# Optimization experiments

Hardware: AMD Instinct MI355X
Metric: run time of the kernel (lower is better)

The kernel has to match this reference:

```python
import jax, jax.numpy as jnp
import numpy as np

B, T, C, H = 128, 256, 384, 6
D = C // H  # head dim = 64


def setup_inputs() -> dict:
    key = jax.random.key(0)
    k1, k2, k3, k4, k5 = jax.random.split(key, 5)
    s = 0.02
    return {
        "x": jax.random.normal(k1, (B, T, C), dtype=jnp.float32),
        "W_qkv": jax.random.normal(k2, (C, 3 * C), dtype=jnp.float32) * s,
        "b_qkv": jax.random.normal(k3, (3 * C,), dtype=jnp.float32) * s,
        "W_proj": jax.random.normal(k4, (C, C), dtype=jnp.float32) * s,
        "b_proj": jax.random.normal(k5, (C,), dtype=jnp.float32) * s,
    }


def reference(x, W_qkv, b_qkv, W_proj, b_proj):
    Bv, Tv, Cv = x.shape
    # fused QKV projection, then split
    qkv = x @ W_qkv + b_qkv                      # [B,T,3C]
    q, k, v = jnp.split(qkv, 3, axis=-1)
    # [B,T,C] -> [B,H,T,D]
    q = q.reshape(Bv, Tv, H, D).transpose(0, 2, 1, 3)
    k = k.reshape(Bv, Tv, H, D).transpose(0, 2, 1, 3)
    v = v.reshape(Bv, Tv, H, D).transpose(0, 2, 1, 3)
    # causal masked scores, scaled by head_dim**-0.5
    scores = jnp.einsum("bhqd,bhkd->bhqk", q, k) * (D ** -0.5)
    causal = jnp.tril(jnp.ones((Tv, Tv), dtype=bool))
    scores = jnp.where(causal, scores, -jnp.inf)
    wt = jax.nn.softmax(scores, axis=-1)
    # dropout layers are identity in eval mode
    out = jnp.einsum("bhqk,bhkd->bhqd", wt, v)   # [B,H,T,D]
    out = out.transpose(0, 2, 1, 3).reshape(Bv, Tv, Cv)
    return out @ W_proj + b_proj
```

## Files before the change

kernel.cpp:

```cpp
#include <hip/hip_runtime.h>

typedef unsigned short u16;
typedef unsigned int u32;
typedef __attribute__((ext_vector_type(4))) float f32x4;
typedef __attribute__((ext_vector_type(8))) __bf16 bf16x8;
typedef __attribute__((ext_vector_type(2))) __bf16 bf16x2;

#define NEGINF (-1e30f)
#define QSCALE 0.18033688011112042f

__device__ __forceinline__ u16 f32_to_bf16(float f) {
  union { float f; unsigned int u; } v;
  v.f = f;
  unsigned int u = v.u;
  u += 0x7fffu + ((u >> 16) & 1u);
  return (u16)(u >> 16);
}

__device__ __forceinline__ u32 pk_bf16(float a, float b) {
  bf16x2 t;
  t.x = (__bf16)a;
  t.y = (__bf16)b;
  return __builtin_bit_cast(u32, t);
}

__device__ __forceinline__ f32x4 mfma_bf16(bf16x8 a, bf16x8 b, f32x4 c) {
  return __builtin_amdgcn_mfma_f32_16x16x32_bf16(a, b, c, 0, 0, 0);
}

#define GLOAD_LDS16(g, l) __builtin_amdgcn_global_load_lds( \
    (const __attribute__((address_space(1))) unsigned int*)(g), \
    (__attribute__((address_space(3))) unsigned int*)(l), 16, 0, 0)

__global__ void k_cvt4(const float4* __restrict__ in, u16* __restrict__ out, int nq) {
  int i = blockIdx.x * blockDim.x + threadIdx.x;
  if (i >= nq) return;
  float4 v = in[i];
  uint2 o;
  o.x = (unsigned int)f32_to_bf16(v.x) | ((unsigned int)f32_to_bf16(v.y) << 16);
  o.y = (unsigned int)f32_to_bf16(v.z) | ((unsigned int)f32_to_bf16(v.w) << 16);
  *(uint2*)(out + (size_t)i * 4) = o;
}

__global__ void k_tcvt(const float* __restrict__ in, u16* __restrict__ out, int K, int N) {
  int idx = blockIdx.x * blockDim.x + threadIdx.x;
  if (idx >= K * N) return;
  int k = idx / N, n = idx - k * N;
  out[(size_t)n * K + k] = f32_to_bf16(in[idx]);
}

__device__ __forceinline__ void gemm256x64(
    const u16* __restrict__ A, const u16* __restrict__ Bt,
    int mBase, int nBase, u16* lsA, u16* lsB,
    f32x4 acc[4][2], int lane, int wv, int wm, int wn) {
  const int l15 = lane & 15;
  size_t aoff[4];
  u32 aldso[4];
#pragma unroll
  for (int jj = 0; jj < 4; ++jj) {
    int c = wv * 256 + jj * 64 + lane;
    int row = c >> 3;
    int kc = (c & 7) ^ (row & 7);
    aoff[jj] = (size_t)(mBase + row) * 384 + kc * 8;
    aldso[jj] = (u32)(wv * 256 + jj * 64) * 8;
  }
  int cb = wv * 64 + lane;
  int brow = cb >> 3;
  size_t boff = (size_t)(nBase + brow) * 384 + (size_t)(((cb & 7) ^ (brow & 7)) * 8);
  u32 bldso = (u32)(wv * 64) * 8;

#define STAGE_T(kt, buf) do { \
  _Pragma("unroll") \
  for (int jj = 0; jj < 4; ++jj) \
    GLOAD_LDS16(A + aoff[jj] + (kt), lsA + (buf) * 16384 + aldso[jj]); \
  GLOAD_LDS16(Bt + boff + (kt), lsB + (buf) * 4096 + bldso); \
  } while (0)

  STAGE_T(0, 0);
#pragma unroll
  for (int t = 0; t < 6; ++t) {
    const int cur = t & 1;
    if (t < 5) {
      STAGE_T((t + 1) * 64, cur ^ 1);
      asm volatile("s_waitcnt vmcnt(5)" ::: "memory");
    } else {
      asm volatile("s_waitcnt vmcnt(0)" ::: "memory");
    }
    __builtin_amdgcn_s_barrier();
    const char* bA = (const char*)(lsA + cur * 16384);
    const char* bB = (const char*)(lsB + cur * 4096);
#pragma unroll
    for (int ks = 0; ks < 2; ++ks) {
      bf16x8 af[4], bfr[2];
#pragma unroll
      for (int i = 0; i < 4; ++i) {
        int row = wm * 64 + i * 16 + l15;
        af[i] = *(const bf16x8*)(bA + row * 128 + (((ks * 4 + (lane >> 4)) ^ (row & 7)) << 4));
      }
#pragma unroll
      for (int j = 0; j < 2; ++j) {
        int row = wn * 32 + j * 16 + l15;
        bfr[j] = *(const bf16x8*)(bB + row * 128 + (((ks * 4 + (lane >> 4)) ^ (row & 7)) << 4));
      }
#pragma unroll
      for (int i = 0; i < 4; ++i)
#pragma unroll
        for (int j = 0; j < 2; ++j)
          acc[i][j] = mfma_bf16(af[i], bfr[j], acc[i][j]);
    }
    __builtin_amdgcn_s_barrier();
  }
#undef STAGE_T
}

__global__ __launch_bounds__(512, 4) void k_qkv(
    const u16* __restrict__ A, const u16* __restrict__ Bt,
    const float* __restrict__ bias,
    u16* __restrict__ Qb, u16* __restrict__ Kb, u16* __restrict__ Vtb) {
  __shared__ __align__(16) u16 lsA[2 * 16384];
  __shared__ __align__(16) u16 lsB[2 * 4096];
  const int tid = threadIdx.x, lane = tid & 63, wv = tid >> 6;
  const int l15 = lane & 15, g = lane >> 4;
  const int wm = wv >> 1, wn = wv & 1;
  const int bid = (int)blockIdx.x;
  const int wgid = (bid & 7) * 288 + (bid >> 3);
  const int mtile = wgid / 18, ntile = wgid % 18;
  const int mBase = mtile * 256, nBase = ntile * 64;
  f32x4 acc[4][2] = {};
  gemm256x64(A, Bt, mBase, nBase, lsA, lsB, acc, lane, wv, wm, wn);

  const int part = nBase / 384;
  const int cbase = nBase - part * 384;
#pragma unroll
  for (int j = 0; j < 2; ++j) {
    int c = cbase + wn * 32 + j * 16 + l15;
    float bv = bias[nBase + wn * 32 + j * 16 + l15];
    int hh = c >> 6, d = c & 63;
    size_t bhh = (size_t)(mtile * 6 + hh);
#pragma unroll
    for (int i = 0; i < 4; ++i) {
      int t0 = wm * 64 + i * 16 + g * 4;
      if (part == 2) {
        uint2 w;
        w.x = pk_bf16(acc[i][j][0] + bv, acc[i][j][1] + bv);
        w.y = pk_bf16(acc[i][j][2] + bv, acc[i][j][3] + bv);
        *(uint2*)(Vtb + (bhh * 64 + d) * 256 + t0) = w;
      } else if (part == 0) {
#pragma unroll
        for (int r = 0; r < 4; ++r)
          Qb[(bhh * 256 + t0 + r) * 64 + d] = f32_to_bf16((acc[i][j][r] + bv) * QSCALE);
      } else {
#pragma unroll
        for (int r = 0; r < 4; ++r)
          Kb[(bhh * 256 + t0 + r) * 64 + d] = f32_to_bf16(acc[i][j][r] + bv);
      }
    }
  }
}

__global__ __launch_bounds__(64, 3) void k_attn(
    const u16* __restrict__ Qb, const u16* __restrict__ Kb,
    const u16* __restrict__ Vtb, u16* __restrict__ Ob) {
  __shared__ __align__(16) u16 lsP[32 * 64];
  const int lane = threadIdx.x;
  const int l15 = lane & 15, g = lane >> 4;
  const int s = 7 - (int)blockIdx.y;
  const int bh = blockIdx.x;
  const int b = bh / 6, h = bh % 6;
  const u16* Qh = Qb + (size_t)bh * (256 * 64);
  const u16* Kh = Kb + (size_t)bh * (256 * 64);
  const u16* Vh = Vtb + (size_t)bh * (64 * 256);
  const int ktiles = (s >> 1) + 1;
  char* pbuf = (char*)lsP;

  bf16x8 qf[2][2];
#pragma unroll
  for (int ks = 0; ks < 2; ++ks)
#pragma unroll
    for (int iq = 0; iq < 2; ++iq)
      qf[ks][iq] = *(const bf16x8*)(Qh + (size_t)(s * 32 + iq * 16 + l15) * 64 + ks * 32 + g * 8);

  f32x4 o[4][2] = {};
  float rl[2] = {0.f, 0.f};

#pragma unroll 1
  for (int kt = 0; kt < ktiles; ++kt) {
    bf16x8 kf[2][4];
#pragma unroll
    for (int ks = 0; ks < 2; ++ks)
#pragma unroll
      for (int jk = 0; jk < 4; ++jk)
        kf[ks][jk] = *(const bf16x8*)(Kh + (size_t)(kt * 64 + jk * 16 + l15) * 64 + ks * 32 + g * 8);

    f32x4 st[4][2] = {};
    __builtin_amdgcn_s_setprio(1);
#pragma unroll
    for (int ks = 0; ks < 2; ++ks)
#pragma unroll
      for (int jk = 0; jk < 4; ++jk)
#pragma unroll
        for (int iq = 0; iq < 2; ++iq)
          st[jk][iq] = mfma_bf16(kf[ks][jk], qf[ks][iq], st[jk][iq]);
    __builtin_amdgcn_s_setprio(0);

    bf16x8 vf[2][4];
#pragma unroll
    for (int ks = 0; ks < 2; ++ks)
#pragma unroll
      for (int jd = 0; jd < 4; ++jd)
        vf[ks][jd] = *(const bf16x8*)(Vh + (size_t)(jd * 16 + l15) * 256 + kt * 64 + ks * 32 + g * 8);

    if (kt == ktiles - 1) {
#pragma unroll
      for (int jk = 0; jk < 4; ++jk)
#pragma unroll
        for (int iq = 0; iq < 2; ++iq)
#pragma unroll
          for (int r = 0; r < 4; ++r)
            if (kt * 64 + jk * 16 + g * 4 + r > s * 32 + iq * 16 + l15)
              st[jk][iq][r] = NEGINF;
    }

    float rs[2] = {0.f, 0.f};
#pragma unroll
    for (int jk = 0; jk < 4; ++jk)
#pragma unroll
      for (int iq = 0; iq < 2; ++iq) {
        float p0 = __builtin_amdgcn_exp2f(st[jk][iq][0]);
        float p1 = __builtin_amdgcn_exp2f(st[jk][iq][1]);
        float p2 = __builtin_amdgcn_exp2f(st[jk][iq][2]);
        float p3 = __builtin_amdgcn_exp2f(st[jk][iq][3]);
        rs[iq] += (p0 + p1) + (p2 + p3);
        int q = iq * 16 + l15;
        int byte = (q * 128 + (jk * 16 + g * 4) * 2) ^ ((q & 7) << 4);
        uint2 w;
        w.x = pk_bf16(p0, p1);
        w.y = pk_bf16(p2, p3);
        *(uint2*)(pbuf + byte) = w;
      }
#pragma unroll
    for (int iq = 0; iq < 2; ++iq) {
      float v = rs[iq];
      v += __shfl_xor(v, 16);
      v += __shfl_xor(v, 32);
      rl[iq] += v;
    }

#pragma unroll
    for (int ks = 0; ks < 2; ++ks) {
      bf16x8 pf[2];
#pragma unroll
      for (int iq = 0; iq < 2; ++iq) {
        int q = iq * 16 + l15;
        pf[iq] = *(const bf16x8*)(pbuf + ((q * 128 + ks * 64 + g * 16) ^ ((q & 7) << 4)));
      }
      __builtin_amdgcn_s_setprio(1);
#pragma unroll
      for (int jd = 0; jd < 4; ++jd)
#pragma unroll
        for (int iq = 0; iq < 2; ++iq)
          o[jd][iq] = mfma_bf16(vf[ks][jd], pf[iq], o[jd][iq]);
      __builtin_amdgcn_s_setprio(0);
    }
  }

#pragma unroll
  for (int iq = 0; iq < 2; ++iq) {
    float inv = 1.0f / rl[iq];
    int q = iq * 16 + l15;
#pragma unroll
    for (int jd = 0; jd < 4; ++jd) {
      uint2 w;
      w.x = pk_bf16(o[jd][iq][0] * inv, o[jd][iq][1] * inv);
      w.y = pk_bf16(o[jd][iq][2] * inv, o[jd][iq][3] * inv);
      int byte = (q * 128 + jd * 32 + g * 8) ^ ((q & 7) << 4);
      *(uint2*)(pbuf + byte) = w;
    }
  }
  asm volatile("s_waitcnt lgkmcnt(0)" ::: "memory");
#pragma unroll
  for (int rep = 0; rep < 4; ++rep) {
    int row = rep * 8 + (lane >> 3);
    int c = lane & 7;
    uint4 v = *(const uint4*)(pbuf + row * 128 + ((c ^ (row & 7)) * 16));
    int t = s * 32 + row;
    *(uint4*)(Ob + ((size_t)(b * 256 + t)) * 384 + h * 64 + c * 8) = v;
  }
}

__global__ __launch_bounds__(512, 4) void k_proj(
    const u16* __restrict__ A, const u16* __restrict__ Bt,
    const float* __restrict__ bias, float* __restrict__ out) {
  __shared__ __align__(16) u16 lsA[2 * 16384];
  __shared__ __align__(16) u16 lsB[2 * 4096];
  const int tid = threadIdx.x, lane = tid & 63, wv = tid >> 6;
  const int l15 = lane & 15, g = lane >> 4;
  const int wm = wv >> 1, wn = wv & 1;
  const int bid = (int)blockIdx.x;
  const int wgid = (bid & 7) * 96 + (bid >> 3);
  const int mtile = wgid / 6, ntile = wgid % 6;
  const int mBase = mtile * 256, nBase = ntile * 64;
  f32x4 acc[4][2] = {};
  gemm256x64(A, Bt, mBase, nBase, lsA, lsB, acc, lane, wv, wm, wn);
#pragma unroll
  for (int j = 0; j < 2; ++j) {
    int col = nBase + wn * 32 + j * 16 + l15;
    float bv = bias[col];
#pragma unroll
    for (int i = 0; i < 4; ++i) {
      int m0 = mBase + wm * 64 + i * 16 + g * 4;
#pragma unroll
      for (int r = 0; r < 4; ++r)
        out[(size_t)(m0 + r) * 384 + col] = acc[i][j][r] + bv;
    }
  }
}

extern "C" void kernel_launch(void* const* d_in, const int* in_sizes, int n_in,
                              void* d_out, int out_size, void* d_ws, size_t ws_size,
                              hipStream_t stream) {
  const float* x     = (const float*)d_in[0];
  const float* Wqkv  = (const float*)d_in[1];
  const float* bqkv  = (const float*)d_in[2];
  const float* Wproj = (const float*)d_in[3];
  const float* bproj = (const float*)d_in[4];
  float* out = (float*)d_out;

  char* ws = (char*)d_ws;
  u16* xb     = (u16*)(ws);
  u16* wqkvb  = (u16*)(ws + 25165824);
  u16* wprojb = (u16*)(ws + 26050560);
  u16* Qb     = (u16*)(ws + 26345472);
  u16* Kb     = (u16*)(ws + 51511296);
  u16* Vtb    = (u16*)(ws + 76677120);
  u16* Ob     = (u16*)(ws + 101842944);

  k_cvt4<<<12288, 256, 0, stream>>>((const float4*)x, xb, 3145728);
  k_tcvt<<<1728, 256, 0, stream>>>(Wqkv, wqkvb, 384, 1152);
  k_tcvt<<<576, 256, 0, stream>>>(Wproj, wprojb, 384, 384);
  k_qkv<<<2304, 512, 0, stream>>>(xb, wqkvb, bqkv, Qb, Kb, Vtb);
  k_attn<<<dim3(768, 8), 64, 0, stream>>>(Qb, Kb, Vtb, Ob);
  k_proj<<<768, 512, 0, stream>>>(Ob, wprojb, bproj, out);
}
```

Baseline: 122.3 us.

## Fuse x fp32-to-bf16 conversion into QKV GEMM and shrink GEMM tiles

Removes the standalone x conversion kernel. The QKV GEMM now loads fp32 x into registers, converts it to bf16 and writes it to swizzled LDS, overlapped with the MFMA work on the other buffer. This avoids writing and re-reading a 25MB bf16 copy of x. Both GEMMs move from 256x64 tiles with 512 threads to 128x64 tiles with 256 threads, which doubles the grid. The cost is register-staged A loads with a full vmcnt(0) wait each step, instead of direct global-to-LDS loads.

Measured after the change: 191.5 us. 56.6% more time.

```diff
diff --git a/kernel.cpp b/kernel.cpp
--- a/kernel.cpp
+++ b/kernel.cpp
@@ -32,16 +32,6 @@
     (const __attribute__((address_space(1))) unsigned int*)(g), \
     (__attribute__((address_space(3))) unsigned int*)(l), 16, 0, 0)
 
-__global__ void k_cvt4(const float4* __restrict__ in, u16* __restrict__ out, int nq) {
-  int i = blockIdx.x * blockDim.x + threadIdx.x;
-  if (i >= nq) return;
-  float4 v = in[i];
-  uint2 o;
-  o.x = (unsigned int)f32_to_bf16(v.x) | ((unsigned int)f32_to_bf16(v.y) << 16);
-  o.y = (unsigned int)f32_to_bf16(v.z) | ((unsigned int)f32_to_bf16(v.w) << 16);
-  *(uint2*)(out + (size_t)i * 4) = o;
-}
-
 __global__ void k_tcvt(const float* __restrict__ in, u16* __restrict__ out, int K, int N) {
   int idx = blockIdx.x * blockDim.x + threadIdx.x;
   if (idx >= K * N) return;
@@ -49,110 +39,130 @@
   out[(size_t)n * K + k] = f32_to_bf16(in[idx]);
 }
 
-__device__ __forceinline__ void gemm256x64(
-    const u16* __restrict__ A, const u16* __restrict__ Bt,
-    int mBase, int nBase, u16* lsA, u16* lsB,
-    f32x4 acc[4][2], int lane, int wv, int wm, int wn) {
-  const int l15 = lane & 15;
-  size_t aoff[4];
-  u32 aldso[4];
-#pragma unroll
-  for (int jj = 0; jj < 4; ++jj) {
-    int c = wv * 256 + jj * 64 + lane;
-    int row = c >> 3;
-    int kc = (c & 7) ^ (row & 7);
-    aoff[jj] = (size_t)(mBase + row) * 384 + kc * 8;
-    aldso[jj] = (u32)(wv * 256 + jj * 64) * 8;
-  }
-  int cb = wv * 64 + lane;
-  int brow = cb >> 3;
-  size_t boff = (size_t)(nBase + brow) * 384 + (size_t)(((cb & 7) ^ (brow & 7)) * 8);
-  u32 bldso = (u32)(wv * 64) * 8;
-
-#define STAGE_T(kt, buf) do { \
-  _Pragma("unroll") \
-  for (int jj = 0; jj < 4; ++jj) \
-    GLOAD_LDS16(A + aoff[jj] + (kt), lsA + (buf) * 16384 + aldso[jj]); \
-  GLOAD_LDS16(Bt + boff + (kt), lsB + (buf) * 4096 + bldso); \
-  } while (0)
-
-  STAGE_T(0, 0);
-#pragma unroll
-  for (int t = 0; t < 6; ++t) {
-    const int cur = t & 1;
-    if (t < 5) {
-      STAGE_T((t + 1) * 64, cur ^ 1);
-      asm volatile("s_waitcnt vmcnt(5)" ::: "memory");
-    } else {
-      asm volatile("s_waitcnt vmcnt(0)" ::: "memory");
-    }
-    __builtin_amdgcn_s_barrier();
-    const char* bA = (const char*)(lsA + cur * 16384);
-    const char* bB = (const char*)(lsB + cur * 4096);
-#pragma unroll
-    for (int ks = 0; ks < 2; ++ks) {
-      bf16x8 af[4], bfr[2];
-#pragma unroll
-      for (int i = 0; i < 4; ++i) {
-        int row = wm * 64 + i * 16 + l15;
-        af[i] = *(const bf16x8*)(bA + row * 128 + (((ks * 4 + (lane >> 4)) ^ (row & 7)) << 4));
-      }
-#pragma unroll
-      for (int j = 0; j < 2; ++j) {
-        int row = wn * 32 + j * 16 + l15;
-        bfr[j] = *(const bf16x8*)(bB + row * 128 + (((ks * 4 + (lane >> 4)) ^ (row & 7)) << 4));
-      }
-#pragma unroll
-      for (int i = 0; i < 4; ++i)
-#pragma unroll
-        for (int j = 0; j < 2; ++j)
-          acc[i][j] = mfma_bf16(af[i], bfr[j], acc[i][j]);
-    }
-    __builtin_amdgcn_s_barrier();
-  }
-#undef STAGE_T
-}
-
-__global__ __launch_bounds__(512, 4) void k_qkv(
-    const u16* __restrict__ A, const u16* __restrict__ Bt,
+__global__ __launch_bounds__(256, 3) void k_qkv(
+    const float* __restrict__ x, const u16* __restrict__ Bt,
     const float* __restrict__ bias,
     u16* __restrict__ Qb, u16* __restrict__ Kb, u16* __restrict__ Vtb) {
-  __shared__ __align__(16) u16 lsA[2 * 16384];
+  __shared__ __align__(16) u16 lsA[2 * 8192];
   __shared__ __align__(16) u16 lsB[2 * 4096];
   const int tid = threadIdx.x, lane = tid & 63, wv = tid >> 6;
   const int l15 = lane & 15, g = lane >> 4;
   const int wm = wv >> 1, wn = wv & 1;
   const int bid = (int)blockIdx.x;
-  const int wgid = (bid & 7) * 288 + (bid >> 3);
+  const int wgid = (bid & 7) * 576 + (bid >> 3);
   const int mtile = wgid / 18, ntile = wgid % 18;
-  const int mBase = mtile * 256, nBase = ntile * 64;
+  const int mBase = mtile * 128, nBase = ntile * 64;
+
+  const int arow = tid >> 1, ahalf = tid & 1;
+  const float* aptr = x + (size_t)(mBase + arow) * 384 + ahalf * 32;
+  u32 awbyte[4];
+#pragma unroll
+  for (int q = 0; q < 4; ++q) {
+    int kc = ahalf * 4 + q;
+    awbyte[q] = (u32)(arow * 128 + ((kc ^ (arow & 7)) << 4));
+  }
+  size_t boff[2]; u32 bldso[2];
+#pragma unroll
+  for (int jj = 0; jj < 2; ++jj) {
+    int c = jj * 256 + tid;
+    int row = c >> 3, kc = (c & 7) ^ (row & 7);
+    boff[jj] = (size_t)(nBase + row) * 384 + kc * 8;
+    bldso[jj] = (u32)c * 8;
+  }
+
   f32x4 acc[4][2] = {};
-  gemm256x64(A, Bt, mBase, nBase, lsA, lsB, acc, lane, wv, wm, wn);
-
-  const int part = nBase / 384;
-  const int cbase = nBase - part * 384;
+  float4 fA[8];
+
+#pragma unroll
+  for (int q = 0; q < 8; ++q)
+    fA[q] = *(const float4*)(aptr + (q >> 1) * 8 + (q & 1) * 4);
+#pragma unroll
+  for (int jj = 0; jj < 2; ++jj)
+    GLOAD_LDS16(Bt + boff[jj], lsB + bldso[jj]);
+  asm volatile("s_waitcnt vmcnt(0)" ::: "memory");
+#pragma unroll
+  for (int q = 0; q < 4; ++q) {
+    uint4 w;
+    w.x = pk_bf16(fA[2*q].x, fA[2*q].y);
+    w.y = pk_bf16(fA[2*q].z, fA[2*q].w);
+    w.z = pk_bf16(fA[2*q+1].x, fA[2*q+1].y);
+    w.w = pk_bf16(fA[2*q+1].z, fA[2*q+1].w);
+    *(uint4*)((char*)lsA + awbyte[q]) = w;
+  }
+  __syncthreads();
+
+#pragma unroll
+  for (int t = 0; t < 6; ++t) {
+    const int cur = t & 1, nxt = cur ^ 1;
+    if (t < 5) {
+#pragma unroll
+      for (int q = 0; q < 8; ++q)
+        fA[q] = *(const float4*)(aptr + (t + 1) * 64 + (q >> 1) * 8 + (q & 1) * 4);
+#pragma unroll
+      for (int jj = 0; jj < 2; ++jj)
+        GLOAD_LDS16(Bt + boff[jj] + (t + 1) * 64, lsB + nxt * 4096 + bldso[jj]);
+    }
+    const char* bA = (const char*)lsA + cur * 16384;
+    const char* bB = (const char*)lsB + cur * 8192;
+#pragma unroll
+    for (int ks = 0; ks < 2; ++ks) {
+      bf16x8 af[4], bfr[2];
+#pragma unroll
+      for (int i = 0; i < 4; ++i) {
+        int row = wm * 64 + i * 16 + l15;
+        af[i] = *(const bf16x8*)(bA + row * 128 + (((ks * 4 + g) ^ (row & 7)) << 4));
+      }
+#pragma unroll
+      for (int j = 0; j < 2; ++j) {
+        int row = wn * 32 + j * 16 + l15;
+        bfr[j] = *(const bf16x8*)(bB + row * 128 + (((ks * 4 + g) ^ (row & 7)) << 4));
+      }
+#pragma unroll
+      for (int i = 0; i < 4; ++i)
+#pragma unroll
+        for (int j = 0; j < 2; ++j)
+          acc[i][j] = mfma_bf16(af[i], bfr[j], acc[i][j]);
+    }
+    if (t < 5) {
+      asm volatile("s_waitcnt vmcnt(0)" ::: "memory");
+#pragma unroll
+      for (int q = 0; q < 4; ++q) {
+        uint4 w;
+        w.x = pk_bf16(fA[2*q].x, fA[2*q].y);
+        w.y = pk_bf16(fA[2*q].z, fA[2*q].w);
+        w.z = pk_bf16(fA[2*q+1].x, fA[2*q+1].y);
+        w.w = pk_bf16(fA[2*q+1].z, fA[2*q+1].w);
+        *(uint4*)((char*)lsA + nxt * 16384 + awbyte[q]) = w;
+      }
+    }
+    __syncthreads();
+  }
+
+  const int part = ntile / 6;
+  const int cbase = (ntile % 6) * 64;
 #pragma unroll
   for (int j = 0; j < 2; ++j) {
     int c = cbase + wn * 32 + j * 16 + l15;
     float bv = bias[nBase + wn * 32 + j * 16 + l15];
     int hh = c >> 6, d = c & 63;
-    size_t bhh = (size_t)(mtile * 6 + hh);
 #pragma unroll
     for (int i = 0; i < 4; ++i) {
-      int t0 = wm * 64 + i * 16 + g * 4;
+      int m0 = mBase + wm * 64 + i * 16 + g * 4;
+      int bb = m0 >> 8, tt = m0 & 255;
+      size_t bhh = (size_t)(bb * 6 + hh);
       if (part == 2) {
         uint2 w;
         w.x = pk_bf16(acc[i][j][0] + bv, acc[i][j][1] + bv);
         w.y = pk_bf16(acc[i][j][2] + bv, acc[i][j][3] + bv);
-        *(uint2*)(Vtb + (bhh * 64 + d) * 256 + t0) = w;
+        *(uint2*)(Vtb + (bhh * 64 + d) * 256 + tt) = w;
       } else if (part == 0) {
 #pragma unroll
         for (int r = 0; r < 4; ++r)
-          Qb[(bhh * 256 + t0 + r) * 64 + d] = f32_to_bf16((acc[i][j][r] + bv) * QSCALE);
+          Qb[(bhh * 256 + tt + r) * 64 + d] = f32_to_bf16((acc[i][j][r] + bv) * QSCALE);
       } else {
 #pragma unroll
         for (int r = 0; r < 4; ++r)
-          Kb[(bhh * 256 + t0 + r) * 64 + d] = f32_to_bf16(acc[i][j][r] + bv);
+          Kb[(bhh * 256 + tt + r) * 64 + d] = f32_to_bf16(acc[i][j][r] + bv);
       }
     }
   }
@@ -288,20 +298,82 @@
   }
 }
 
-__global__ __launch_bounds__(512, 4) void k_proj(
+__global__ __launch_bounds__(256, 3) void k_proj(
     const u16* __restrict__ A, const u16* __restrict__ Bt,
     const float* __restrict__ bias, float* __restrict__ out) {
-  __shared__ __align__(16) u16 lsA[2 * 16384];
+  __shared__ __align__(16) u16 lsA[2 * 8192];
   __shared__ __align__(16) u16 lsB[2 * 4096];
   const int tid = threadIdx.x, lane = tid & 63, wv = tid >> 6;
   const int l15 = lane & 15, g = lane >> 4;
   const int wm = wv >> 1, wn = wv & 1;
   const int bid = (int)blockIdx.x;
-  const int wgid = (bid & 7) * 96 + (bid >> 3);
+  const int wgid = (bid & 7) * 192 + (bid >> 3);
   const int mtile = wgid / 6, ntile = wgid % 6;
-  const int mBase = mtile * 256, nBase = ntile * 64;
+  const int mBase = mtile * 128, nBase = ntile * 64;
+
+  size_t aoff[4]; u32 aldso[4];
+#pragma unroll
+  for (int jj = 0; jj < 4; ++jj) {
+    int c = jj * 256 + tid;
+    int row = c >> 3, kc = (c & 7) ^ (row & 7);
+    aoff[jj] = (size_t)(mBase + row) * 384 + kc * 8;
+    aldso[jj] = (u32)c * 8;
+  }
+  size_t boff[2]; u32 bldso[2];
+#pragma unroll
+  for (int jj = 0; jj < 2; ++jj) {
+    int c = jj * 256 + tid;
+    int row = c >> 3, kc = (c & 7) ^ (row & 7);
+    boff[jj] = (size_t)(nBase + row) * 384 + kc * 8;
+    bldso[jj] = (u32)c * 8;
+  }
+
+#define STAGE_P(kt, buf) do { \
+  _Pragma("unroll") \
+  for (int jj = 0; jj < 4; ++jj) \
+    GLOAD_LDS16(A + aoff[jj] + (kt), lsA + (buf) * 8192 + aldso[jj]); \
+  _Pragma("unroll") \
+  for (int jj = 0; jj < 2; ++jj) \
+    GLOAD_LDS16(Bt + boff[jj] + (kt), lsB + (buf) * 4096 + bldso[jj]); \
+  } while (0)
+
   f32x4 acc[4][2] = {};
-  gemm256x64(A, Bt, mBase, nBase, lsA, lsB, acc, lane, wv, wm, wn);
+  STAGE_P(0, 0);
+#pragma unroll
+  for (int t = 0; t < 6; ++t) {
+    const int cur = t & 1;
+    if (t < 5) {
+      STAGE_P((t + 1) * 64, cur ^ 1);
+      asm volatile("s_waitcnt vmcnt(6)" ::: "memory");
+    } else {
+      asm volatile("s_waitcnt vmcnt(0)" ::: "memory");
+    }
+    __builtin_amdgcn_s_barrier();
+    const char* bA = (const char*)lsA + cur * 16384;
+    const char* bB = (const char*)lsB + cur * 8192;
+#pragma unroll
+    for (int ks = 0; ks < 2; ++ks) {
+      bf16x8 af[4], bfr[2];
+#pragma unroll
+      for (int i = 0; i < 4; ++i) {
+        int row = wm * 64 + i * 16 + l15;
+        af[i] = *(const bf16x8*)(bA + row * 128 + (((ks * 4 + g) ^ (row & 7)) << 4));
+      }
+#pragma unroll
+      for (int j = 0; j < 2; ++j) {
+        int row = wn * 32 + j * 16 + l15;
+        bfr[j] = *(const bf16x8*)(bB + row * 128 + (((ks * 4 + g) ^ (row & 7)) << 4));
+      }
+#pragma unroll
+      for (int i = 0; i < 4; ++i)
+#pragma unroll
+        for (int j = 0; j < 2; ++j)
+          acc[i][j] = mfma_bf16(af[i], bfr[j], acc[i][j]);
+    }
+    __builtin_amdgcn_s_barrier();
+  }
+#undef STAGE_P
+
 #pragma unroll
   for (int j = 0; j < 2; ++j) {
     int col = nBase + wn * 32 + j * 16 + l15;
@@ -327,18 +399,16 @@
   float* out = (float*)d_out;
 
   char* ws = (char*)d_ws;
-  u16* xb     = (u16*)(ws);
-  u16* wqkvb  = (u16*)(ws + 25165824);
-  u16* wprojb = (u16*)(ws + 26050560);
-  u16* Qb     = (u16*)(ws + 26345472);
-  u16* Kb     = (u16*)(ws + 51511296);
-  u16* Vtb    = (u16*)(ws + 76677120);
-  u16* Ob     = (u16*)(ws + 101842944);
-
-  k_cvt4<<<12288, 256, 0, stream>>>((const float4*)x, xb, 3145728);
+  u16* wqkvb  = (u16*)(ws);
+  u16* wprojb = (u16*)(ws + 884736);
+  u16* Qb     = (u16*)(ws + 1179648);
+  u16* Kb     = (u16*)(ws + 26345472);
+  u16* Vtb    = (u16*)(ws + 51511296);
+  u16* Ob     = (u16*)(ws + 76677120);
+
   k_tcvt<<<1728, 256, 0, stream>>>(Wqkv, wqkvb, 384, 1152);
   k_tcvt<<<576, 256, 0, stream>>>(Wproj, wprojb, 384, 384);
-  k_qkv<<<2304, 512, 0, stream>>>(xb, wqkvb, bqkv, Qb, Kb, Vtb);
+  k_qkv<<<4608, 256, 0, stream>>>(x, wqkvb, bqkv, Qb, Kb, Vtb);
   k_attn<<<dim3(768, 8), 64, 0, stream>>>(Qb, Kb, Vtb, Ob);
-  k_proj<<<768, 512, 0, stream>>>(Ob, wprojb, bproj, out);
-}
+  k_proj<<<1536, 256, 0, stream>>>(Ob, wprojb, bproj, out);
+}
```

## Replace LDS-staged GEMM with direct global-to-register double-buffered MFMA loads

Applied to the files above, without the earlier changes.

Both GEMM kernels (QKV and output projection) drop the shared-memory staging via global_load_lds. Each wave now loads its MFMA fragments straight from global memory into registers, double-buffered across the six K-steps with vmcnt waits, and raises wave priority around the MFMA bursts. Blocks shrink from 512 threads on a 256x64 tile to 256 threads on a 128x64 tile, doubling the grid. This removes LDS traffic and barriers, but gives up cross-wave data sharing: global loads are now uncoalesced 16-byte row fragments and the same data is read redundantly, and register pressure rises.

New measurement: 270.6 us. 2.21x slower.

```diff
diff --git a/kernel.cpp b/kernel.cpp
--- a/kernel.cpp
+++ b/kernel.cpp
@@ -27,10 +27,6 @@
 __device__ __forceinline__ f32x4 mfma_bf16(bf16x8 a, bf16x8 b, f32x4 c) {
   return __builtin_amdgcn_mfma_f32_16x16x32_bf16(a, b, c, 0, 0, 0);
 }
-
-#define GLOAD_LDS16(g, l) __builtin_amdgcn_global_load_lds( \
-    (const __attribute__((address_space(1))) unsigned int*)(g), \
-    (__attribute__((address_space(3))) unsigned int*)(l), 16, 0, 0)
 
 __global__ void k_cvt4(const float4* __restrict__ in, u16* __restrict__ out, int nq) {
   int i = blockIdx.x * blockDim.x + threadIdx.x;
@@ -49,110 +45,83 @@
   out[(size_t)n * K + k] = f32_to_bf16(in[idx]);
 }
 
-__device__ __forceinline__ void gemm256x64(
-    const u16* __restrict__ A, const u16* __restrict__ Bt,
-    int mBase, int nBase, u16* lsA, u16* lsB,
-    f32x4 acc[4][2], int lane, int wv, int wm, int wn) {
-  const int l15 = lane & 15;
-  size_t aoff[4];
-  u32 aldso[4];
-#pragma unroll
-  for (int jj = 0; jj < 4; ++jj) {
-    int c = wv * 256 + jj * 64 + lane;
-    int row = c >> 3;
-    int kc = (c & 7) ^ (row & 7);
-    aoff[jj] = (size_t)(mBase + row) * 384 + kc * 8;
-    aldso[jj] = (u32)(wv * 256 + jj * 64) * 8;
-  }
-  int cb = wv * 64 + lane;
-  int brow = cb >> 3;
-  size_t boff = (size_t)(nBase + brow) * 384 + (size_t)(((cb & 7) ^ (brow & 7)) * 8);
-  u32 bldso = (u32)(wv * 64) * 8;
-
-#define STAGE_T(kt, buf) do { \
+#define VMCNT(n) asm volatile("s_waitcnt vmcnt(" #n ")" ::: "memory")
+
+#define LOADT(kt, af, bf) do { \
   _Pragma("unroll") \
-  for (int jj = 0; jj < 4; ++jj) \
-    GLOAD_LDS16(A + aoff[jj] + (kt), lsA + (buf) * 16384 + aldso[jj]); \
-  GLOAD_LDS16(Bt + boff + (kt), lsB + (buf) * 4096 + bldso); \
-  } while (0)
-
-  STAGE_T(0, 0);
-#pragma unroll
-  for (int t = 0; t < 6; ++t) {
-    const int cur = t & 1;
-    if (t < 5) {
-      STAGE_T((t + 1) * 64, cur ^ 1);
-      asm volatile("s_waitcnt vmcnt(5)" ::: "memory");
-    } else {
-      asm volatile("s_waitcnt vmcnt(0)" ::: "memory");
-    }
-    __builtin_amdgcn_s_barrier();
-    const char* bA = (const char*)(lsA + cur * 16384);
-    const char* bB = (const char*)(lsB + cur * 4096);
-#pragma unroll
-    for (int ks = 0; ks < 2; ++ks) {
-      bf16x8 af[4], bfr[2];
-#pragma unroll
-      for (int i = 0; i < 4; ++i) {
-        int row = wm * 64 + i * 16 + l15;
-        af[i] = *(const bf16x8*)(bA + row * 128 + (((ks * 4 + (lane >> 4)) ^ (row & 7)) << 4));
-      }
-#pragma unroll
-      for (int j = 0; j < 2; ++j) {
-        int row = wn * 32 + j * 16 + l15;
-        bfr[j] = *(const bf16x8*)(bB + row * 128 + (((ks * 4 + (lane >> 4)) ^ (row & 7)) << 4));
-      }
-#pragma unroll
-      for (int i = 0; i < 4; ++i)
-#pragma unroll
-        for (int j = 0; j < 2; ++j)
-          acc[i][j] = mfma_bf16(af[i], bfr[j], acc[i][j]);
-    }
-    __builtin_amdgcn_s_barrier();
-  }
-#undef STAGE_T
-}
-
-__global__ __launch_bounds__(512, 4) void k_qkv(
+  for (int ks = 0; ks < 2; ++ks) { \
+    _Pragma("unroll") \
+    for (int i = 0; i < 4; ++i) \
+      af[ks * 4 + i] = *(const bf16x8*)(pa + (size_t)i * (16 * 384) + (kt) * 64 + ks * 32); \
+    _Pragma("unroll") \
+    for (int j = 0; j < 2; ++j) \
+      bf[ks * 2 + j] = *(const bf16x8*)(pb + (size_t)j * (16 * 384) + (kt) * 64 + ks * 32); \
+  } \
+} while (0)
+
+#define MFMA_SET(af, bf) do { \
+  __builtin_amdgcn_s_setprio(1); \
+  _Pragma("unroll") \
+  for (int ks = 0; ks < 2; ++ks) \
+    _Pragma("unroll") \
+    for (int i = 0; i < 4; ++i) \
+      _Pragma("unroll") \
+      for (int j = 0; j < 2; ++j) \
+        acc[i][j] = mfma_bf16(af[ks * 4 + i], bf[ks * 2 + j], acc[i][j]); \
+  __builtin_amdgcn_s_setprio(0); \
+} while (0)
+
+__global__ __launch_bounds__(256, 3) void k_qkv(
     const u16* __restrict__ A, const u16* __restrict__ Bt,
     const float* __restrict__ bias,
     u16* __restrict__ Qb, u16* __restrict__ Kb, u16* __restrict__ Vtb) {
-  __shared__ __align__(16) u16 lsA[2 * 16384];
-  __shared__ __align__(16) u16 lsB[2 * 4096];
   const int tid = threadIdx.x, lane = tid & 63, wv = tid >> 6;
   const int l15 = lane & 15, g = lane >> 4;
   const int wm = wv >> 1, wn = wv & 1;
   const int bid = (int)blockIdx.x;
-  const int wgid = (bid & 7) * 288 + (bid >> 3);
+  const int wgid = (bid & 7) * 576 + (bid >> 3);
   const int mtile = wgid / 18, ntile = wgid % 18;
-  const int mBase = mtile * 256, nBase = ntile * 64;
+  const int mBase = mtile * 128, nBase = ntile * 64;
+
+  const u16* pa = A + (size_t)(mBase + wm * 64 + l15) * 384 + g * 8;
+  const u16* pb = Bt + (size_t)(nBase + wn * 32 + l15) * 384 + g * 8;
+
   f32x4 acc[4][2] = {};
-  gemm256x64(A, Bt, mBase, nBase, lsA, lsB, acc, lane, wv, wm, wn);
-
-  const int part = nBase / 384;
-  const int cbase = nBase - part * 384;
+  bf16x8 afA[8], bfA[4], afB[8], bfB[4];
+
+  LOADT(0, afA, bfA);
+  LOADT(1, afB, bfB); VMCNT(12); MFMA_SET(afA, bfA);
+  LOADT(2, afA, bfA); VMCNT(12); MFMA_SET(afB, bfB);
+  LOADT(3, afB, bfB); VMCNT(12); MFMA_SET(afA, bfA);
+  LOADT(4, afA, bfA); VMCNT(12); MFMA_SET(afB, bfB);
+  LOADT(5, afB, bfB); VMCNT(12); MFMA_SET(afA, bfA);
+  VMCNT(0);           MFMA_SET(afB, bfB);
+
+  const int part = ntile / 6;
+  const int cbase = (ntile % 6) * 64;
 #pragma unroll
   for (int j = 0; j < 2; ++j) {
     int c = cbase + wn * 32 + j * 16 + l15;
     float bv = bias[nBase + wn * 32 + j * 16 + l15];
     int hh = c >> 6, d = c & 63;
-    size_t bhh = (size_t)(mtile * 6 + hh);
 #pragma unroll
     for (int i = 0; i < 4; ++i) {
-      int t0 = wm * 64 + i * 16 + g * 4;
+      int m0 = mBase + wm * 64 + i * 16 + g * 4;
+      int bb = m0 >> 8, tt = m0 & 255;
+      size_t bhh = (size_t)(bb * 6 + hh);
       if (part == 2) {
         uint2 w;
         w.x = pk_bf16(acc[i][j][0] + bv, acc[i][j][1] + bv);
         w.y = pk_bf16(acc[i][j][2] + bv, acc[i][j][3] + bv);
-        *(uint2*)(Vtb + (bhh * 64 + d) * 256 + t0) = w;
+        *(uint2*)(Vtb + (bhh * 64 + d) * 256 + tt) = w;
       } else if (part == 0) {
 #pragma unroll
         for (int r = 0; r < 4; ++r)
-          Qb[(bhh * 256 + t0 + r) * 64 + d] = f32_to_bf16((acc[i][j][r] + bv) * QSCALE);
+          Qb[(bhh * 256 + tt + r) * 64 + d] = f32_to_bf16((acc[i][j][r] + bv) * QSCALE);
       } else {
 #pragma unroll
         for (int r = 0; r < 4; ++r)
-          Kb[(bhh * 256 + t0 + r) * 64 + d] = f32_to_bf16(acc[i][j][r] + bv);
+          Kb[(bhh * 256 + tt + r) * 64 + d] = f32_to_bf16(acc[i][j][r] + bv);
       }
     }
   }
@@ -288,20 +257,31 @@
   }
 }
 
-__global__ __launch_bounds__(512, 4) void k_proj(
+__global__ __launch_bounds__(256, 3) void k_proj(
     const u16* __restrict__ A, const u16* __restrict__ Bt,
     const float* __restrict__ bias, float* __restrict__ out) {
-  __shared__ __align__(16) u16 lsA[2 * 16384];
-  __shared__ __align__(16) u16 lsB[2 * 4096];
   const int tid = threadIdx.x, lane = tid & 63, wv = tid >> 6;
   const int l15 = lane & 15, g = lane >> 4;
   const int wm = wv >> 1, wn = wv & 1;
   const int bid = (int)blockIdx.x;
-  const int wgid = (bid & 7) * 96 + (bid >> 3);
+  const int wgid = (bid & 7) * 192 + (bid >> 3);
   const int mtile = wgid / 6, ntile = wgid % 6;
-  const int mBase = mtile * 256, nBase = ntile * 64;
+  const int mBase = mtile * 128, nBase = ntile * 64;
+
+  const u16* pa = A + (size_t)(mBase + wm * 64 + l15) * 384 + g * 8;
+  const u16* pb = Bt + (size_t)(nBase + wn * 32 + l15) * 384 + g * 8;
+
   f32x4 acc[4][2] = {};
-  gemm256x64(A, Bt, mBase, nBase, lsA, lsB, acc, lane, wv, wm, wn);
+  bf16x8 afA[8], bfA[4], afB[8], bfB[4];
+
+  LOADT(0, afA, bfA);
+  LOADT(1, afB, bfB); VMCNT(12); MFMA_SET(afA, bfA);
+  LOADT(2, afA, bfA); VMCNT(12); MFMA_SET(afB, bfB);
+  LOADT(3, afB, bfB); VMCNT(12); MFMA_SET(afA, bfA);
+  LOADT(4, afA, bfA); VMCNT(12); MFMA_SET(afB, bfB);
+  LOADT(5, afB, bfB); VMCNT(12); MFMA_SET(afA, bfA);
+  VMCNT(0);           MFMA_SET(afB, bfB);
+
 #pragma unroll
   for (int j = 0; j < 2; ++j) {
     int col = nBase + wn * 32 + j * 16 + l15;
@@ -338,7 +318,7 @@
   k_cvt4<<<12288, 256, 0, stream>>>((const float4*)x, xb, 3145728);
   k_tcvt<<<1728, 256, 0, stream>>>(Wqkv, wqkvb, 384, 1152);
   k_tcvt<<<576, 256, 0, stream>>>(Wproj, wprojb, 384, 384);
-  k_qkv<<<2304, 512, 0, stream>>>(xb, wqkvb, bqkv, Qb, Kb, Vtb);
+  k_qkv<<<4608, 256, 0, stream>>>(xb, wqkvb, bqkv, Qb, Kb, Vtb);
   k_attn<<<dim3(768, 8), 64, 0, stream>>>(Qb, Kb, Vtb, Ob);
-  k_proj<<<768, 512, 0, stream>>>(Ob, wprojb, bproj, out);
-}
+  k_proj<<<1536, 256, 0, stream>>>(Ob, wprojb, bproj, out);
+}
```

## Switch QKV and projection GEMMs to 128x128 tiles with single-buffered LDS

Applied to the files above, without the earlier changes.

Replaces the 256x64 double-buffered GEMM tile (512 threads) with a square 128x128 tile computed by 4 waves, each producing a 64x64 sub-block with 4x4 MFMA accumulators. The square tile raises arithmetic intensity per LDS byte and halves the LDS footprint, so more blocks can be resident per CU. In exchange it drops the double-buffered prefetch: global-to-LDS loads are no longer overlapped with MFMA, and each k-step now waits on synchronous barriers. It also adds s_setprio around the MFMA bursts. The epilogues are rewritten for the new tile geometry, including per-column Q/K/V part selection.

Result: no change. 121.9 us (-0.4%).

```diff
diff --git a/kernel.cpp b/kernel.cpp
--- a/kernel.cpp
+++ b/kernel.cpp
@@ -49,110 +49,96 @@
   out[(size_t)n * K + k] = f32_to_bf16(in[idx]);
 }
 
-__device__ __forceinline__ void gemm256x64(
+__device__ __forceinline__ void gemm128sq(
     const u16* __restrict__ A, const u16* __restrict__ Bt,
     int mBase, int nBase, u16* lsA, u16* lsB,
-    f32x4 acc[4][2], int lane, int wv, int wm, int wn) {
-  const int l15 = lane & 15;
-  size_t aoff[4];
-  u32 aldso[4];
+    f32x4 acc[4][4], int lane, int wv) {
+  const int l15 = lane & 15, g = lane >> 4;
+  const int wm = wv >> 1, wn = wv & 1;
+  size_t aoff[4], boff[4];
+  u32 ldso[4];
 #pragma unroll
   for (int jj = 0; jj < 4; ++jj) {
-    int c = wv * 256 + jj * 64 + lane;
+    int c = jj * 256 + wv * 64 + lane;
     int row = c >> 3;
     int kc = (c & 7) ^ (row & 7);
     aoff[jj] = (size_t)(mBase + row) * 384 + kc * 8;
-    aldso[jj] = (u32)(wv * 256 + jj * 64) * 8;
-  }
-  int cb = wv * 64 + lane;
-  int brow = cb >> 3;
-  size_t boff = (size_t)(nBase + brow) * 384 + (size_t)(((cb & 7) ^ (brow & 7)) * 8);
-  u32 bldso = (u32)(wv * 64) * 8;
-
-#define STAGE_T(kt, buf) do { \
-  _Pragma("unroll") \
-  for (int jj = 0; jj < 4; ++jj) \
-    GLOAD_LDS16(A + aoff[jj] + (kt), lsA + (buf) * 16384 + aldso[jj]); \
-  GLOAD_LDS16(Bt + boff + (kt), lsB + (buf) * 4096 + bldso); \
-  } while (0)
-
-  STAGE_T(0, 0);
-#pragma unroll
+    boff[jj] = (size_t)(nBase + row) * 384 + kc * 8;
+    ldso[jj] = (u32)c * 8;
+  }
+#pragma unroll 1
   for (int t = 0; t < 6; ++t) {
-    const int cur = t & 1;
-    if (t < 5) {
-      STAGE_T((t + 1) * 64, cur ^ 1);
-      asm volatile("s_waitcnt vmcnt(5)" ::: "memory");
-    } else {
-      asm volatile("s_waitcnt vmcnt(0)" ::: "memory");
-    }
-    __builtin_amdgcn_s_barrier();
-    const char* bA = (const char*)(lsA + cur * 16384);
-    const char* bB = (const char*)(lsB + cur * 4096);
+#pragma unroll
+    for (int jj = 0; jj < 4; ++jj) {
+      GLOAD_LDS16(A + aoff[jj] + t * 64, lsA + ldso[jj]);
+      GLOAD_LDS16(Bt + boff[jj] + t * 64, lsB + ldso[jj]);
+    }
+    __syncthreads();
 #pragma unroll
     for (int ks = 0; ks < 2; ++ks) {
-      bf16x8 af[4], bfr[2];
+      bf16x8 af[4], bfr[4];
 #pragma unroll
       for (int i = 0; i < 4; ++i) {
         int row = wm * 64 + i * 16 + l15;
-        af[i] = *(const bf16x8*)(bA + row * 128 + (((ks * 4 + (lane >> 4)) ^ (row & 7)) << 4));
-      }
-#pragma unroll
-      for (int j = 0; j < 2; ++j) {
-        int row = wn * 32 + j * 16 + l15;
-        bfr[j] = *(const bf16x8*)(bB + row * 128 + (((ks * 4 + (lane >> 4)) ^ (row & 7)) << 4));
-      }
+        af[i] = *(const bf16x8*)((const char*)lsA + row * 128 + (((ks * 4 + g) ^ (row & 7)) << 4));
+      }
+#pragma unroll
+      for (int j = 0; j < 4; ++j) {
+        int row = wn * 64 + j * 16 + l15;
+        bfr[j] = *(const bf16x8*)((const char*)lsB + row * 128 + (((ks * 4 + g) ^ (row & 7)) << 4));
+      }
+      __builtin_amdgcn_s_setprio(1);
 #pragma unroll
       for (int i = 0; i < 4; ++i)
 #pragma unroll
-        for (int j = 0; j < 2; ++j)
+        for (int j = 0; j < 4; ++j)
           acc[i][j] = mfma_bf16(af[i], bfr[j], acc[i][j]);
-    }
-    __builtin_amdgcn_s_barrier();
-  }
-#undef STAGE_T
-}
-
-__global__ __launch_bounds__(512, 4) void k_qkv(
+      __builtin_amdgcn_s_setprio(0);
+    }
+    __syncthreads();
+  }
+}
+
+__global__ __launch_bounds__(256, 3) void k_qkv(
     const u16* __restrict__ A, const u16* __restrict__ Bt,
     const float* __restrict__ bias,
     u16* __restrict__ Qb, u16* __restrict__ Kb, u16* __restrict__ Vtb) {
-  __shared__ __align__(16) u16 lsA[2 * 16384];
-  __shared__ __align__(16) u16 lsB[2 * 4096];
+  __shared__ __align__(16) u16 lsA[8192];
+  __shared__ __align__(16) u16 lsB[8192];
   const int tid = threadIdx.x, lane = tid & 63, wv = tid >> 6;
   const int l15 = lane & 15, g = lane >> 4;
   const int wm = wv >> 1, wn = wv & 1;
   const int bid = (int)blockIdx.x;
   const int wgid = (bid & 7) * 288 + (bid >> 3);
-  const int mtile = wgid / 18, ntile = wgid % 18;
-  const int mBase = mtile * 256, nBase = ntile * 64;
-  f32x4 acc[4][2] = {};
-  gemm256x64(A, Bt, mBase, nBase, lsA, lsB, acc, lane, wv, wm, wn);
-
-  const int part = nBase / 384;
-  const int cbase = nBase - part * 384;
-#pragma unroll
-  for (int j = 0; j < 2; ++j) {
-    int c = cbase + wn * 32 + j * 16 + l15;
-    float bv = bias[nBase + wn * 32 + j * 16 + l15];
+  const int mBase = (wgid / 9) * 128, nBase = (wgid % 9) * 128;
+  f32x4 acc[4][4] = {};
+  gemm128sq(A, Bt, mBase, nBase, lsA, lsB, acc, lane, wv);
+
+#pragma unroll
+  for (int j = 0; j < 4; ++j) {
+    int col = nBase + wn * 64 + j * 16 + l15;
+    float bv = bias[col];
+    int part = col / 384;
+    int c = col - part * 384;
     int hh = c >> 6, d = c & 63;
-    size_t bhh = (size_t)(mtile * 6 + hh);
 #pragma unroll
     for (int i = 0; i < 4; ++i) {
-      int t0 = wm * 64 + i * 16 + g * 4;
+      int m0 = mBase + wm * 64 + i * 16 + g * 4;
+      int bb = m0 >> 8, tt = m0 & 255;
+      size_t bhh = (size_t)(bb * 6 + hh);
       if (part == 2) {
         uint2 w;
         w.x = pk_bf16(acc[i][j][0] + bv, acc[i][j][1] + bv);
         w.y = pk_bf16(acc[i][j][2] + bv, acc[i][j][3] + bv);
-        *(uint2*)(Vtb + (bhh * 64 + d) * 256 + t0) = w;
+        *(uint2*)(Vtb + (bhh * 64 + d) * 256 + tt) = w;
       } else if (part == 0) {
 #pragma unroll
         for (int r = 0; r < 4; ++r)
-          Qb[(bhh * 256 + t0 + r) * 64 + d] = f32_to_bf16((acc[i][j][r] + bv) * QSCALE);
+          Qb[(bhh * 256 + tt + r) * 64 + d] = f32_to_bf16((acc[i][j][r] + bv) * QSCALE);
       } else {
 #pragma unroll
         for (int r = 0; r < 4; ++r)
-          Kb[(bhh * 256 + t0 + r) * 64 + d] = f32_to_bf16(acc[i][j][r] + bv);
+          Kb[(bhh * 256 + tt + r) * 64 + d] = f32_to_bf16(acc[i][j][r] + bv);
       }
     }
   }
@@ -288,23 +274,22 @@
   }
 }
 
-__global__ __launch_bounds__(512, 4) void k_proj(
+__global__ __launch_bounds__(256, 3) void k_proj(
     const u16* __restrict__ A, const u16* __restrict__ Bt,
     const float* __restrict__ bias, float* __restrict__ out) {
-  __shared__ __align__(16) u16 lsA[2 * 16384];
-  __shared__ __align__(16) u16 lsB[2 * 4096];
+  __shared__ __align__(16) u16 lsA[8192];
+  __shared__ __align__(16) u16 lsB[8192];
   const int tid = threadIdx.x, lane = tid & 63, wv = tid >> 6;
   const int l15 = lane & 15, g = lane >> 4;
   const int wm = wv >> 1, wn = wv & 1;
   const int bid = (int)blockIdx.x;
   const int wgid = (bid & 7) * 96 + (bid >> 3);
-  const int mtile = wgid / 6, ntile = wgid % 6;
-  const int mBase = mtile * 256, nBase = ntile * 64;
-  f32x4 acc[4][2] = {};
-  gemm256x64(A, Bt, mBase, nBase, lsA, lsB, acc, lane, wv, wm, wn);
-#pragma unroll
-  for (int j = 0; j < 2; ++j) {
-    int col = nBase + wn * 32 + j * 16 + l15;
+  const int mBase = (wgid / 3) * 128, nBase = (wgid % 3) * 128;
+  f32x4 acc[4][4] = {};
+  gemm128sq(A, Bt, mBase, nBase, lsA, lsB, acc, lane, wv);
+#pragma unroll
+  for (int j = 0; j < 4; ++j) {
+    int col = nBase + wn * 64 + j * 16 + l15;
     float bv = bias[col];
 #pragma unroll
     for (int i = 0; i < 4; ++i) {
@@ -338,7 +323,7 @@
   k_cvt4<<<12288, 256, 0, stream>>>((const float4*)x, xb, 3145728);
   k_tcvt<<<1728, 256, 0, stream>>>(Wqkv, wqkvb, 384, 1152);
   k_tcvt<<<576, 256, 0, stream>>>(Wproj, wprojb, 384, 384);
-  k_qkv<<<2304, 512, 0, stream>>>(xb, wqkvb, bqkv, Qb, Kb, Vtb);
+  k_qkv<<<2304, 256, 0, stream>>>(xb, wqkvb, bqkv, Qb, Kb, Vtb);
   k_attn<<<dim3(768, 8), 64, 0, stream>>>(Qb, Kb, Vtb, Ob);
-  k_proj<<<768, 512, 0, stream>>>(Ob, wprojb, bproj, out);
-}
+  k_proj<<<768, 256, 0, stream>>>(Ob, wprojb, bproj, out);
+}
```
